# Optimization experiments

Measured on AMD Instinct MI355X. Metric: run time of the kernel, lower is better.

## Reference

```python
import math
import jax, jax.numpy as jnp
import numpy as np

BS, T, D_MODEL, H = 4, 1024, 1024, 16
D_K = D_MODEL // H


def setup_inputs() -> dict:
    key = jax.random.key(0)
    ks = jax.random.split(key, 16)
    s = 0.02  # weight init scale
    return {
        "q": jax.random.normal(ks[0], (BS, T, D_MODEL), jnp.float32),
        "k": jax.random.normal(ks[1], (BS, T, D_MODEL), jnp.float32),
        "v": jax.random.normal(ks[2], (BS, T, D_MODEL), jnp.float32),
        "pos_emb": jax.random.normal(ks[3], (1, T, D_MODEL), jnp.float32),
        "mask": jnp.ones((BS, T, T), jnp.int32),
        "Wq": jax.random.normal(ks[4], (D_MODEL, D_MODEL), jnp.float32) * s,
        "bq": jax.random.normal(ks[5], (D_MODEL,), jnp.float32) * s,
        "Wk": jax.random.normal(ks[6], (D_MODEL, D_MODEL), jnp.float32) * s,
        "bk": jax.random.normal(ks[7], (D_MODEL,), jnp.float32) * s,
        "Wv": jax.random.normal(ks[8], (D_MODEL, D_MODEL), jnp.float32) * s,
        "bv": jax.random.normal(ks[9], (D_MODEL,), jnp.float32) * s,
        "Wp": jax.random.normal(ks[10], (D_MODEL, D_MODEL), jnp.float32) * s,
        "pos_bias_u": jax.random.normal(ks[11], (H, D_K), jnp.float32) * s,
        "pos_bias_v": jax.random.normal(ks[12], (H, D_K), jnp.float32) * s,
        "Wo": jax.random.normal(ks[13], (D_MODEL, D_MODEL), jnp.float32) * s,
        "bo": jax.random.normal(ks[14], (D_MODEL,), jnp.float32) * s,
    }


def rel_shift(x):
    # x: [b, h, T, P]; Transformer-XL relative shift via pad+reshape
    b, h, t, p = x.shape
    x = jnp.pad(x, ((0, 0), (0, 0), (0, 0), (1, 0)))  # [b,h,T,P+1]
    x = x.reshape(b, h, p + 1, t)[:, :, 1:, :]
    return x.reshape(b, h, t, p)


def reference(q, k, v, pos_emb, mask, Wq, bq, Wk, bk, Wv, bv, Wp,
              pos_bias_u, pos_bias_v, Wo, bo):
    bs, t, d_model = q.shape
    h, d_k = pos_bias_u.shape
    # projections (torch Linear: x @ W.T + b)
    qh = (q @ Wq.T + bq).reshape(bs, t, h, d_k)                      # [b,t,h,d]
    kh = (k @ Wk.T + bk).reshape(bs, t, h, d_k).transpose(0, 2, 1, 3)  # [b,h,s,d]
    vh = (v @ Wv.T + bv).reshape(bs, t, h, d_k).transpose(0, 2, 1, 3)  # [b,h,s,d]
    p = (pos_emb @ Wp.T).reshape(pos_emb.shape[0], -1, h, d_k).transpose(0, 2, 1, 3)  # [1,h,P,d]
    q_u = (qh + pos_bias_u).transpose(0, 2, 1, 3)  # [b,h,t,d]
    q_v = (qh + pos_bias_v).transpose(0, 2, 1, 3)  # [b,h,t,d]
    matrix_ac = jnp.einsum('bhtd,bhsd->bhts', q_u, kh)
    matrix_bd = jnp.einsum('bhtd,hpd->bhtp', q_v, p[0])
    matrix_bd = rel_shift(matrix_bd)
    scores = (matrix_ac + matrix_bd) / math.sqrt(d_k)
    m = mask[:, None, :, :]  # broadcast over heads
    attn = jax.nn.softmax(jnp.where(m == 0, jnp.float32(-10000.0), scores), axis=-1)
    out_h = jnp.einsum('bhts,bhsd->bhtd', attn, vh)
    concat = out_h.transpose(0, 2, 1, 3).reshape(bs, t, d_model)
    output = concat @ Wo.T + bo
    return (output, attn)
```

## Files before the change

kernel.cpp:

```cpp
#include <hip/hip_runtime.h>

typedef _Float16 f16;
typedef __attribute__((ext_vector_type(8))) _Float16 f16x8;
typedef __attribute__((ext_vector_type(4))) float f32x4;

#define LDK 40
#define SST 1032
#define BST 72

__device__ __forceinline__ void stage_f16g(const f16* __restrict__ src, int ld, f16* dst) {
    int t = threadIdx.x;
    int row = t >> 2;
    int c0 = (t & 3) * 8;
    *(f16x8*)(dst + row * LDK + c0) = *(const f16x8*)(src + (size_t)row * ld + c0);
}

__device__ __forceinline__ void mma_step(const f16* As, const f16* Bs, int m_off, int n_off,
                                         f32x4 acc[2][2]) {
    int lane = threadIdx.x & 63;
    int r = lane & 15;
    int kq = (lane >> 4) * 8;
    f16x8 a0 = *(const f16x8*)(As + (m_off + r) * LDK + kq);
    f16x8 a1 = *(const f16x8*)(As + (m_off + 16 + r) * LDK + kq);
    f16x8 b0 = *(const f16x8*)(Bs + (n_off + r) * LDK + kq);
    f16x8 b1 = *(const f16x8*)(Bs + (n_off + 16 + r) * LDK + kq);
    acc[0][0] = __builtin_amdgcn_mfma_f32_16x16x32_f16(a0, b0, acc[0][0], 0, 0, 0);
    acc[0][1] = __builtin_amdgcn_mfma_f32_16x16x32_f16(a0, b1, acc[0][1], 0, 0, 0);
    acc[1][0] = __builtin_amdgcn_mfma_f32_16x16x32_f16(a1, b0, acc[1][0], 0, 0, 0);
    acc[1][1] = __builtin_amdgcn_mfma_f32_16x16x32_f16(a1, b1, acc[1][1], 0, 0, 0);
}

#define GEMM_PROLOGUE()                                         \
    __shared__ __align__(16) f16 As[64 * LDK];                  \
    __shared__ __align__(16) f16 Bs[64 * LDK];                  \
    const int w = threadIdx.x >> 6;                             \
    const int m_off = (w & 1) * 32, n_off = (w >> 1) * 32;      \
    const int lane = threadIdx.x & 63;                          \
    f32x4 zero = {0.f, 0.f, 0.f, 0.f};                          \
    f32x4 acc[2][2] = {{zero, zero}, {zero, zero}};

__global__ __launch_bounds__(256) void cvt_all(
    const float* __restrict__ q, const float* __restrict__ k, const float* __restrict__ v,
    const float* __restrict__ pe, const float* __restrict__ Wq, const float* __restrict__ Wk,
    const float* __restrict__ Wv, const float* __restrict__ Wp, const float* __restrict__ Wo,
    f16* __restrict__ dst) {
    const int seg = blockIdx.y;
    const float* srcs[9] = {q, k, v, pe, Wq, Wk, Wv, Wp, Wo};
    const int sz = (seg < 3) ? 4194304 : 1048576;
    const size_t off = (seg < 3) ? (size_t)seg * 4194304
                                 : (size_t)12582912 + (size_t)(seg - 3) * 1048576;
    const size_t i0 = ((size_t)blockIdx.x * 256 + threadIdx.x) * 16;
    if (i0 >= (size_t)sz) return;
    const float* s = srcs[seg] + i0;
    f16* d = dst + off + i0;
#pragma unroll
    for (int half = 0; half < 2; ++half) {
        float4 u = *(const float4*)(s + half * 8);
        float4 w = *(const float4*)(s + half * 8 + 4);
        f16x8 h;
        h[0] = (f16)u.x; h[1] = (f16)u.y; h[2] = (f16)u.z; h[3] = (f16)u.w;
        h[4] = (f16)w.x; h[5] = (f16)w.y; h[6] = (f16)w.z; h[7] = (f16)w.w;
        *(f16x8*)(d + half * 8) = h;
    }
}

__global__ __launch_bounds__(256) void proj_qkv(
    const f16* __restrict__ qf, const f16* __restrict__ kf, const f16* __restrict__ vf,
    const f16* __restrict__ Wqf, const f16* __restrict__ Wkf, const f16* __restrict__ Wvf,
    const float* __restrict__ bq, const float* __restrict__ bk, const float* __restrict__ bv,
    const float* __restrict__ pbu, const float* __restrict__ pbv,
    f16* __restrict__ q_u, f16* __restrict__ q_v, f16* __restrict__ kh,
    f16* __restrict__ vh) {
    GEMM_PROLOGUE();
    const int z = blockIdx.z;
    const f16* A = (z == 0) ? qf : (z == 1) ? kf : vf;
    const f16* W = (z == 0) ? Wqf : (z == 1) ? Wkf : Wvf;
    const float* bias = (z == 0) ? bq : (z == 1) ? bk : bv;
    const int m0 = blockIdx.y * 64, n0 = blockIdx.x * 64;
    for (int k0 = 0; k0 < 1024; k0 += 32) {
        stage_f16g(A + (size_t)m0 * 1024 + k0, 1024, As);
        stage_f16g(W + (size_t)n0 * 1024 + k0, 1024, Bs);
        __syncthreads();
        mma_step(As, Bs, m_off, n_off, acc);
        __syncthreads();
    }
#pragma unroll
    for (int mt = 0; mt < 2; ++mt)
#pragma unroll
        for (int nt = 0; nt < 2; ++nt)
#pragma unroll
            for (int rr = 0; rr < 4; ++rr) {
                int m = m0 + m_off + mt * 16 + (lane >> 4) * 4 + rr;
                int n = n0 + n_off + nt * 16 + (lane & 15);
                float base = acc[mt][nt][rr] + bias[n];
                int b = m >> 10, t = m & 1023, h = n >> 6, d = n & 63;
                size_t idx = ((size_t)((b * 16 + h) * 1024 + t)) * 64 + d;
                if (z == 0) {
                    q_u[idx] = (f16)(base + pbu[n]);
                    q_v[idx] = (f16)(base + pbv[n]);
                } else if (z == 1) {
                    kh[idx] = (f16)base;
                } else {
                    vh[idx] = (f16)base;
                }
            }
}

__global__ __launch_bounds__(256) void proj_p(const f16* __restrict__ A,
                                              const f16* __restrict__ W,
                                              f16* __restrict__ o1) {
    GEMM_PROLOGUE();
    const int m0 = blockIdx.y * 64;
    const int n0 = blockIdx.x * 64;
    for (int k0 = 0; k0 < 1024; k0 += 32) {
        stage_f16g(A + (size_t)m0 * 1024 + k0, 1024, As);
        stage_f16g(W + (size_t)n0 * 1024 + k0, 1024, Bs);
        __syncthreads();
        mma_step(As, Bs, m_off, n_off, acc);
        __syncthreads();
    }
#pragma unroll
    for (int mt = 0; mt < 2; ++mt)
#pragma unroll
        for (int nt = 0; nt < 2; ++nt)
#pragma unroll
            for (int rr = 0; rr < 4; ++rr) {
                int m = m0 + m_off + mt * 16 + (lane >> 4) * 4 + rr;
                int n = n0 + n_off + nt * 16 + (lane & 15);
                int h = n >> 6, d = n & 63;
                o1[((size_t)h * 1024 + m) * 64 + d] = (f16)acc[mt][nt][rr];
            }
}

__global__ __launch_bounds__(256) void transpose_v(const f16* __restrict__ vh,
                                                   f16* __restrict__ vT) {
    __shared__ __align__(16) f16 T[64 * BST];
    const int bh = blockIdx.y;
    const int j0 = blockIdx.x * 64;
    const int t = threadIdx.x;
    const int s = t >> 2, c0 = (t & 3) * 16;
    const f16* src = vh + (size_t)bh * 65536 + (size_t)(j0 + s) * 64;
    *(f16x8*)(T + s * BST + c0) = *(const f16x8*)(src + c0);
    *(f16x8*)(T + s * BST + c0 + 8) = *(const f16x8*)(src + c0 + 8);
    __syncthreads();
    const int d = t >> 2;
    f16x8 o0, o1;
#pragma unroll
    for (int j = 0; j < 8; ++j) {
        o0[j] = T[(c0 + j) * BST + d];
        o1[j] = T[(c0 + 8 + j) * BST + d];
    }
    f16* dst = vT + (size_t)bh * 65536 + (size_t)d * 1024 + j0 + c0;
    *(f16x8*)(dst) = o0;
    *(f16x8*)(dst + 8) = o1;
}

__global__ __launch_bounds__(256, 2) void fused_attn(
    const f16* __restrict__ q_u, const f16* __restrict__ q_v,
    const f16* __restrict__ kh, const f16* __restrict__ pp,
    const f16* __restrict__ vT, const int* __restrict__ mask,
    float* __restrict__ attn, f16* __restrict__ oh) {
    __shared__ __align__(16) f16 Ssc[32 * SST];
    __shared__ __align__(16) f16 Bt[64 * BST];
    __shared__ __align__(16) f16 rawX[1024];
    __shared__ __align__(16) f16 qxrow[64];

    const int bh = blockIdx.y;
    const int b = bh >> 4, h = bh & 15;
    const int i0 = blockIdx.x * 32;
    const int tid = threadIdx.x;
    const int w = tid >> 6;
    const int lane = tid & 63;
    const int m_off = (w & 1) * 16, n_off = (w >> 1) * 32;
    const int fr = lane & 15;
    const int kq = (lane >> 4) * 8;
    const f32x4 zero = {0.f, 0.f, 0.f, 0.f};

    const f16* Qu = q_u + (size_t)bh * 65536;
    const f16* Qv = q_v + (size_t)bh * 65536;
    const f16* Kh = kh + (size_t)bh * 65536;
    const f16* Pp = pp + (size_t)h * 65536;
    const f16* Vt = vT + (size_t)bh * 65536;

    f16x8 qu_f[2], qv_f[2];
#pragma unroll
    for (int ks = 0; ks < 2; ++ks) {
        size_t off = (size_t)(i0 + m_off + fr) * 64 + ks * 32 + kq;
        qu_f[ks] = *(const f16x8*)(Qu + off);
        qv_f[ks] = *(const f16x8*)(Qv + off);
    }
    if (i0 + 32 < 1024 && tid < 8)
        *(f16x8*)(qxrow + tid * 8) = *(const f16x8*)(Qv + (size_t)(i0 + 32) * 64 + tid * 8);

    const int srow = tid >> 2, sc0 = (tid & 3) * 16;
    for (int j0 = 0; j0 < 1024; j0 += 64) {
        {
            const f16* s = Pp + (size_t)(j0 + srow) * 64 + sc0;
            *(f16x8*)(Bt + srow * BST + sc0) = *(const f16x8*)(s);
            *(f16x8*)(Bt + srow * BST + sc0 + 8) = *(const f16x8*)(s + 8);
        }
        __syncthreads();
        f32x4 acc[2] = {zero, zero};
#pragma unroll
        for (int ks = 0; ks < 2; ++ks) {
            f16x8 b0 = *(const f16x8*)(Bt + (n_off + fr) * BST + ks * 32 + kq);
            f16x8 b1 = *(const f16x8*)(Bt + (n_off + 16 + fr) * BST + ks * 32 + kq);
            acc[0] = __builtin_amdgcn_mfma_f32_16x16x32_f16(qv_f[ks], b0, acc[0], 0, 0, 0);
            acc[1] = __builtin_amdgcn_mfma_f32_16x16x32_f16(qv_f[ks], b1, acc[1], 0, 0, 0);
        }
#pragma unroll
        for (int nt = 0; nt < 2; ++nt)
#pragma unroll
            for (int rr = 0; rr < 4; ++rr) {
                int m = m_off + (lane >> 4) * 4 + rr;
                int c = j0 + n_off + nt * 16 + fr;
                Ssc[m * SST + c] = (f16)acc[nt][rr];
            }
        __syncthreads();
    }

    if (i0 + 32 < 1024) {
        int p = tid * 4;
#pragma unroll
        for (int pi = 0; pi < 4; ++pi) {
            const f16* pr = Pp + (size_t)(p + pi) * 64;
            float sacc = 0.f;
#pragma unroll
            for (int c = 0; c < 64; c += 8) {
                f16x8 pv = *(const f16x8*)(pr + c);
                f16x8 qv8 = *(const f16x8*)(qxrow + c);
#pragma unroll
                for (int j = 0; j < 8; ++j) sacc += (float)pv[j] * (float)qv8[j];
            }
            rawX[p + pi] = (f16)sacc;
        }
    }
    __syncthreads();

    {
        const int s0 = lane * 16;
        f16 tmp[8][16];
#pragma unroll
        for (int rr2 = 0; rr2 < 8; ++rr2) {
            int lr = w * 8 + rr2;
            int r = i0 + lr;
#pragma unroll
            for (int j = 0; j < 16; ++j) {
                int s = s0 + j;
                f16 val;
                if (s <= r) val = Ssc[lr * SST + (s + 1023 - r)];
                else if (s == r + 1) val = (f16)0.f;
                else val = (lr == 31) ? rawX[s - r - 2] : Ssc[(lr + 1) * SST + (s - r - 2)];
                tmp[rr2][j] = val;
            }
        }
        __syncthreads();
#pragma unroll
        for (int rr2 = 0; rr2 < 8; ++rr2) {
            int lr = w * 8 + rr2;
            f16x8 o0, o1;
#pragma unroll
            for (int j = 0; j < 8; ++j) { o0[j] = tmp[rr2][j]; o1[j] = tmp[rr2][8 + j]; }
            *(f16x8*)(Ssc + lr * SST + s0) = o0;
            *(f16x8*)(Ssc + lr * SST + s0 + 8) = o1;
        }
    }
    __syncthreads();

    for (int j0 = 0; j0 < 1024; j0 += 64) {
        {
            const f16* s = Kh + (size_t)(j0 + srow) * 64 + sc0;
            *(f16x8*)(Bt + srow * BST + sc0) = *(const f16x8*)(s);
            *(f16x8*)(Bt + srow * BST + sc0 + 8) = *(const f16x8*)(s + 8);
        }
        __syncthreads();
        f32x4 acc[2] = {zero, zero};
#pragma unroll
        for (int ks = 0; ks < 2; ++ks) {
            f16x8 b0 = *(const f16x8*)(Bt + (n_off + fr) * BST + ks * 32 + kq);
            f16x8 b1 = *(const f16x8*)(Bt + (n_off + 16 + fr) * BST + ks * 32 + kq);
            acc[0] = __builtin_amdgcn_mfma_f32_16x16x32_f16(qu_f[ks], b0, acc[0], 0, 0, 0);
            acc[1] = __builtin_amdgcn_mfma_f32_16x16x32_f16(qu_f[ks], b1, acc[1], 0, 0, 0);
        }
#pragma unroll
        for (int nt = 0; nt < 2; ++nt)
#pragma unroll
            for (int rr = 0; rr < 4; ++rr) {
                int m = m_off + (lane >> 4) * 4 + rr;
                int c = j0 + n_off + nt * 16 + fr;
                float sc = ((float)Ssc[m * SST + c] + acc[nt][rr]) * 0.125f;
                Ssc[m * SST + c] = (f16)sc;
            }
        __syncthreads();
    }

    float* Ab = attn + (size_t)bh * 1048576;
    const int* MK = mask + ((size_t)b * 1024 + i0) * 1024;
    for (int rr = 0; rr < 8; ++rr) {
        int lr = w * 8 + rr;
        int c0 = lane * 16;
        f16x8 a0 = *(const f16x8*)(Ssc + lr * SST + c0);
        f16x8 a1 = *(const f16x8*)(Ssc + lr * SST + c0 + 8);
        const int* mrow = MK + (size_t)lr * 1024 + c0;
        int4 mk0 = *(const int4*)mrow;
        int4 mk1 = *(const int4*)(mrow + 4);
        int4 mk2 = *(const int4*)(mrow + 8);
        int4 mk3 = *(const int4*)(mrow + 12);
        int mks[16] = {mk0.x, mk0.y, mk0.z, mk0.w, mk1.x, mk1.y, mk1.z, mk1.w,
                       mk2.x, mk2.y, mk2.z, mk2.w, mk3.x, mk3.y, mk3.z, mk3.w};
        float vals[16];
        float mx = -1e30f;
#pragma unroll
        for (int j = 0; j < 16; ++j) {
            float v = (j < 8) ? (float)a0[j] : (float)a1[j - 8];
            if (mks[j] == 0) v = -10000.0f;
            vals[j] = v;
            mx = fmaxf(mx, v);
        }
#pragma unroll
        for (int off = 32; off > 0; off >>= 1) mx = fmaxf(mx, __shfl_xor(mx, off));
        float sum = 0.f;
#pragma unroll
        for (int j = 0; j < 16; ++j) { vals[j] = __expf(vals[j] - mx); sum += vals[j]; }
#pragma unroll
        for (int off = 32; off > 0; off >>= 1) sum += __shfl_xor(sum, off);
        float il = 1.f / sum;
        float* arow = Ab + (size_t)(i0 + lr) * 1024 + c0;
        float4 f0 = {vals[0] * il, vals[1] * il, vals[2] * il, vals[3] * il};
        float4 f1 = {vals[4] * il, vals[5] * il, vals[6] * il, vals[7] * il};
        float4 f2 = {vals[8] * il, vals[9] * il, vals[10] * il, vals[11] * il};
        float4 f3 = {vals[12] * il, vals[13] * il, vals[14] * il, vals[15] * il};
        *(float4*)(arow) = f0;
        *(float4*)(arow + 4) = f1;
        *(float4*)(arow + 8) = f2;
        *(float4*)(arow + 12) = f3;
        f16x8 p0, p1;
#pragma unroll
        for (int j = 0; j < 8; ++j) {
            p0[j] = (f16)(vals[j] * il);
            p1[j] = (f16)(vals[8 + j] * il);
        }
        *(f16x8*)(Ssc + lr * SST + c0) = p0;
        *(f16x8*)(Ssc + lr * SST + c0 + 8) = p1;
    }

    f32x4 accp[2] = {zero, zero};
    for (int j0 = 0; j0 < 1024; j0 += 64) {
        {
            const f16* s = Vt + (size_t)srow * 1024 + j0 + sc0;
            *(f16x8*)(Bt + srow * BST + sc0) = *(const f16x8*)(s);
            *(f16x8*)(Bt + srow * BST + sc0 + 8) = *(const f16x8*)(s + 8);
        }
        __syncthreads();
#pragma unroll
        for (int ks = 0; ks < 2; ++ks) {
            f16x8 a0 = *(const f16x8*)(Ssc + (m_off + fr) * SST + j0 + ks * 32 + kq);
            f16x8 b0 = *(const f16x8*)(Bt + (n_off + fr) * BST + ks * 32 + kq);
            f16x8 b1 = *(const f16x8*)(Bt + (n_off + 16 + fr) * BST + ks * 32 + kq);
            accp[0] = __builtin_amdgcn_mfma_f32_16x16x32_f16(a0, b0, accp[0], 0, 0, 0);
            accp[1] = __builtin_amdgcn_mfma_f32_16x16x32_f16(a0, b1, accp[1], 0, 0, 0);
        }
        __syncthreads();
    }
#pragma unroll
    for (int nt = 0; nt < 2; ++nt)
#pragma unroll
        for (int rr = 0; rr < 4; ++rr) {
            int t = i0 + m_off + (lane >> 4) * 4 + rr;
            int d = n_off + nt * 16 + fr;
            oh[((size_t)(b * 1024 + t)) * 1024 + h * 64 + d] = (f16)accp[nt][rr];
        }
}

__global__ __launch_bounds__(256) void out_gemm(const f16* __restrict__ A,
                                                const f16* __restrict__ W,
                                                const float* __restrict__ bias,
                                                float* __restrict__ out) {
    GEMM_PROLOGUE();
    const int m0 = blockIdx.y * 64;
    const int n0 = blockIdx.x * 64;
    for (int k0 = 0; k0 < 1024; k0 += 32) {
        stage_f16g(A + (size_t)m0 * 1024 + k0, 1024, As);
        stage_f16g(W + (size_t)n0 * 1024 + k0, 1024, Bs);
        __syncthreads();
        mma_step(As, Bs, m_off, n_off, acc);
        __syncthreads();
    }
#pragma unroll
    for (int mt = 0; mt < 2; ++mt)
#pragma unroll
        for (int nt = 0; nt < 2; ++nt)
#pragma unroll
            for (int rr = 0; rr < 4; ++rr) {
                int m = m0 + m_off + mt * 16 + (lane >> 4) * 4 + rr;
                int n = n0 + n_off + nt * 16 + (lane & 15);
                out[(size_t)m * 1024 + n] = acc[mt][nt][rr] + bias[n];
            }
}

extern "C" void kernel_launch(void* const* d_in, const int* in_sizes, int n_in,
                              void* d_out, int out_size, void* d_ws, size_t ws_size,
                              hipStream_t stream) {
    (void)in_sizes; (void)n_in; (void)out_size; (void)ws_size;
    const float* q   = (const float*)d_in[0];
    const float* k   = (const float*)d_in[1];
    const float* v   = (const float*)d_in[2];
    const float* pe  = (const float*)d_in[3];
    const int*   msk = (const int*)d_in[4];
    const float* Wq  = (const float*)d_in[5];
    const float* bq  = (const float*)d_in[6];
    const float* Wk  = (const float*)d_in[7];
    const float* bk  = (const float*)d_in[8];
    const float* Wv  = (const float*)d_in[9];
    const float* bv  = (const float*)d_in[10];
    const float* Wp  = (const float*)d_in[11];
    const float* pbu = (const float*)d_in[12];
    const float* pbv = (const float*)d_in[13];
    const float* Wo  = (const float*)d_in[14];
    const float* bo  = (const float*)d_in[15];

    char* ws = (char*)d_ws;
    f16* cvt = (f16*)(ws + 0);
    f16* qf  = cvt;
    f16* kf  = cvt + 4194304;
    f16* vf  = cvt + 8388608;
    f16* pef = cvt + 12582912;
    f16* Wqf = cvt + 13631488;
    f16* Wkf = cvt + 14680064;
    f16* Wvf = cvt + 15728640;
    f16* Wpf = cvt + 16777216;
    f16* Wof = cvt + 17825792;

    f16* q_u = (f16*)(ws + 37748736);
    f16* q_v = (f16*)(ws + 46137344);
    f16* kh  = (f16*)(ws + 54525952);
    f16* vh  = (f16*)(ws + 62914560);
    f16* pp  = (f16*)(ws + 71303168);
    f16* oh  = (f16*)(ws + 73400320);
    f16* vT  = (f16*)(ws + 81788928);

    float* out  = (float*)d_out;
    float* attn = out + 4194304;

    dim3 blk(256);
    cvt_all<<<dim3(1024, 9), blk, 0, stream>>>(q, k, v, pe, Wq, Wk, Wv, Wp, Wo, cvt);
    proj_qkv<<<dim3(16, 64, 3), blk, 0, stream>>>(qf, kf, vf, Wqf, Wkf, Wvf, bq, bk, bv,
                                                  pbu, pbv, q_u, q_v, kh, vh);
    proj_p<<<dim3(16, 16), blk, 0, stream>>>(pef, Wpf, pp);
    transpose_v<<<dim3(16, 64), blk, 0, stream>>>(vh, vT);
    fused_attn<<<dim3(32, 64), blk, 0, stream>>>(q_u, q_v, kh, pp, vT, msk, attn, oh);
    out_gemm<<<dim3(16, 64), blk, 0, stream>>>(oh, Wof, bo, out);
}
```

Before: 684.8 us.

## Register-prefetch GEMM tiles and fold rel_shift into score scatter

Adds register double-buffering to all GEMM k-loops and to the P, K and V tile loops in the attention kernel, so the next global tile load is issued before the current MFMA step. It also scatters the positional scores directly into their rel-shifted positions, replacing the separate gather pass, its extra barriers and the rawX buffer. Softmax column mapping changes to two strided halves per lane for better LDS and global coalescing. The shifted-scatter indexing is intricate and could hide correctness edge cases.

```diff
diff --git a/kernel.cpp b/kernel.cpp
--- a/kernel.cpp
+++ b/kernel.cpp
@@ -8,11 +8,17 @@
 #define SST 1032
 #define BST 72
 
-__device__ __forceinline__ void stage_f16g(const f16* __restrict__ src, int ld, f16* dst) {
+__device__ __forceinline__ f16x8 ld_half(const f16* __restrict__ src, int ld) {
     int t = threadIdx.x;
     int row = t >> 2;
     int c0 = (t & 3) * 8;
-    *(f16x8*)(dst + row * LDK + c0) = *(const f16x8*)(src + (size_t)row * ld + c0);
+    return *(const f16x8*)(src + (size_t)row * ld + c0);
+}
+__device__ __forceinline__ void st_half(f16* dst, f16x8 v) {
+    int t = threadIdx.x;
+    int row = t >> 2;
+    int c0 = (t & 3) * 8;
+    *(f16x8*)(dst + row * LDK + c0) = v;
 }
 
 __device__ __forceinline__ void mma_step(const f16* As, const f16* Bs, int m_off, int n_off,
@@ -38,6 +44,23 @@
     const int lane = threadIdx.x & 63;                          \
     f32x4 zero = {0.f, 0.f, 0.f, 0.f};                          \
     f32x4 acc[2][2] = {{zero, zero}, {zero, zero}};
+
+#define GEMM_KLOOP(Abase, Wbase)                                        \
+    {                                                                   \
+        f16x8 ra = ld_half((Abase), 1024);                              \
+        f16x8 rb = ld_half((Wbase), 1024);                              \
+        for (int k0 = 0; k0 < 1024; k0 += 32) {                         \
+            st_half(As, ra);                                            \
+            st_half(Bs, rb);                                            \
+            __syncthreads();                                            \
+            if (k0 + 32 < 1024) {                                       \
+                ra = ld_half((Abase) + k0 + 32, 1024);                  \
+                rb = ld_half((Wbase) + k0 + 32, 1024);                  \
+            }                                                           \
+            mma_step(As, Bs, m_off, n_off, acc);                        \
+            __syncthreads();                                            \
+        }                                                               \
+    }
 
 __global__ __launch_bounds__(256) void cvt_all(
     const float* __restrict__ q, const float* __restrict__ k, const float* __restrict__ v,
@@ -77,13 +100,7 @@
     const f16* W = (z == 0) ? Wqf : (z == 1) ? Wkf : Wvf;
     const float* bias = (z == 0) ? bq : (z == 1) ? bk : bv;
     const int m0 = blockIdx.y * 64, n0 = blockIdx.x * 64;
-    for (int k0 = 0; k0 < 1024; k0 += 32) {
-        stage_f16g(A + (size_t)m0 * 1024 + k0, 1024, As);
-        stage_f16g(W + (size_t)n0 * 1024 + k0, 1024, Bs);
-        __syncthreads();
-        mma_step(As, Bs, m_off, n_off, acc);
-        __syncthreads();
-    }
+    GEMM_KLOOP(A + (size_t)m0 * 1024, W + (size_t)n0 * 1024);
 #pragma unroll
     for (int mt = 0; mt < 2; ++mt)
 #pragma unroll
@@ -112,13 +129,7 @@
     GEMM_PROLOGUE();
     const int m0 = blockIdx.y * 64;
     const int n0 = blockIdx.x * 64;
-    for (int k0 = 0; k0 < 1024; k0 += 32) {
-        stage_f16g(A + (size_t)m0 * 1024 + k0, 1024, As);
-        stage_f16g(W + (size_t)n0 * 1024 + k0, 1024, Bs);
-        __syncthreads();
-        mma_step(As, Bs, m_off, n_off, acc);
-        __syncthreads();
-    }
+    GEMM_KLOOP(A + (size_t)m0 * 1024, W + (size_t)n0 * 1024);
 #pragma unroll
     for (int mt = 0; mt < 2; ++mt)
 #pragma unroll
@@ -162,7 +173,6 @@
     float* __restrict__ attn, f16* __restrict__ oh) {
     __shared__ __align__(16) f16 Ssc[32 * SST];
     __shared__ __align__(16) f16 Bt[64 * BST];
-    __shared__ __align__(16) f16 rawX[1024];
     __shared__ __align__(16) f16 qxrow[64];
 
     const int bh = blockIdx.y;
@@ -193,119 +203,127 @@
         *(f16x8*)(qxrow + tid * 8) = *(const f16x8*)(Qv + (size_t)(i0 + 32) * 64 + tid * 8);
 
     const int srow = tid >> 2, sc0 = (tid & 3) * 16;
-    for (int j0 = 0; j0 < 1024; j0 += 64) {
+
+    {
+        f16x8 pf0, pf1;
         {
-            const f16* s = Pp + (size_t)(j0 + srow) * 64 + sc0;
-            *(f16x8*)(Bt + srow * BST + sc0) = *(const f16x8*)(s);
-            *(f16x8*)(Bt + srow * BST + sc0 + 8) = *(const f16x8*)(s + 8);
-        }
-        __syncthreads();
-        f32x4 acc[2] = {zero, zero};
-#pragma unroll
-        for (int ks = 0; ks < 2; ++ks) {
-            f16x8 b0 = *(const f16x8*)(Bt + (n_off + fr) * BST + ks * 32 + kq);
-            f16x8 b1 = *(const f16x8*)(Bt + (n_off + 16 + fr) * BST + ks * 32 + kq);
-            acc[0] = __builtin_amdgcn_mfma_f32_16x16x32_f16(qv_f[ks], b0, acc[0], 0, 0, 0);
-            acc[1] = __builtin_amdgcn_mfma_f32_16x16x32_f16(qv_f[ks], b1, acc[1], 0, 0, 0);
-        }
-#pragma unroll
-        for (int nt = 0; nt < 2; ++nt)
-#pragma unroll
-            for (int rr = 0; rr < 4; ++rr) {
-                int m = m_off + (lane >> 4) * 4 + rr;
-                int c = j0 + n_off + nt * 16 + fr;
-                Ssc[m * SST + c] = (f16)acc[nt][rr];
-            }
-        __syncthreads();
+            const f16* s = Pp + (size_t)srow * 64 + sc0;
+            pf0 = *(const f16x8*)(s);
+            pf1 = *(const f16x8*)(s + 8);
+        }
+        for (int j0 = 0; j0 < 1024; j0 += 64) {
+            *(f16x8*)(Bt + srow * BST + sc0) = pf0;
+            *(f16x8*)(Bt + srow * BST + sc0 + 8) = pf1;
+            __syncthreads();
+            if (j0 + 64 < 1024) {
+                const f16* s = Pp + (size_t)(j0 + 64 + srow) * 64 + sc0;
+                pf0 = *(const f16x8*)(s);
+                pf1 = *(const f16x8*)(s + 8);
+            }
+            f32x4 acc[2] = {zero, zero};
+#pragma unroll
+            for (int ks = 0; ks < 2; ++ks) {
+                f16x8 b0 = *(const f16x8*)(Bt + (n_off + fr) * BST + ks * 32 + kq);
+                f16x8 b1 = *(const f16x8*)(Bt + (n_off + 16 + fr) * BST + ks * 32 + kq);
+                acc[0] = __builtin_amdgcn_mfma_f32_16x16x32_f16(qv_f[ks], b0, acc[0], 0, 0, 0);
+                acc[1] = __builtin_amdgcn_mfma_f32_16x16x32_f16(qv_f[ks], b1, acc[1], 0, 0, 0);
+            }
+#pragma unroll
+            for (int nt = 0; nt < 2; ++nt)
+#pragma unroll
+                for (int rr = 0; rr < 4; ++rr) {
+                    int m = m_off + (lane >> 4) * 4 + rr;
+                    int p = j0 + n_off + nt * 16 + fr;
+                    int pr = p + i0 + m;
+                    f16 v = (f16)acc[nt][rr];
+                    if (pr >= 1023) {
+                        Ssc[m * SST + (pr - 1023)] = v;
+                    } else if (m > 0) {
+                        Ssc[(m - 1) * SST + (pr + 1)] = v;
+                    }
+                }
+            __syncthreads();
+        }
+    }
+
+    if (tid < 32) {
+        int c = i0 + tid + 1;
+        if (c < 1024) Ssc[tid * SST + c] = (f16)0.f;
     }
 
     if (i0 + 32 < 1024) {
-        int p = tid * 4;
-#pragma unroll
-        for (int pi = 0; pi < 4; ++pi) {
-            const f16* pr = Pp + (size_t)(p + pi) * 64;
-            float sacc = 0.f;
-#pragma unroll
-            for (int c = 0; c < 64; c += 8) {
-                f16x8 pv = *(const f16x8*)(pr + c);
-                f16x8 qv8 = *(const f16x8*)(qxrow + c);
-#pragma unroll
-                for (int j = 0; j < 8; ++j) sacc += (float)pv[j] * (float)qv8[j];
-            }
-            rawX[p + pi] = (f16)sacc;
-        }
-    }
-    __syncthreads();
+        int base = tid * 4;
+        if (base + i0 + 33 <= 1023) {
+#pragma unroll
+            for (int pi = 0; pi < 4; ++pi) {
+                int p = base + pi;
+                int s = p + i0 + 33;
+                if (s <= 1023) {
+                    const f16* pr = Pp + (size_t)p * 64;
+                    float sacc = 0.f;
+#pragma unroll
+                    for (int c = 0; c < 64; c += 8) {
+                        f16x8 pv = *(const f16x8*)(pr + c);
+                        f16x8 qv8 = *(const f16x8*)(qxrow + c);
+#pragma unroll
+                        for (int j = 0; j < 8; ++j) sacc += (float)pv[j] * (float)qv8[j];
+                    }
+                    Ssc[31 * SST + s] = (f16)sacc;
+                }
+            }
+        }
+    }
 
     {
-        const int s0 = lane * 16;
-        f16 tmp[8][16];
-#pragma unroll
-        for (int rr2 = 0; rr2 < 8; ++rr2) {
-            int lr = w * 8 + rr2;
-            int r = i0 + lr;
-#pragma unroll
-            for (int j = 0; j < 16; ++j) {
-                int s = s0 + j;
-                f16 val;
-                if (s <= r) val = Ssc[lr * SST + (s + 1023 - r)];
-                else if (s == r + 1) val = (f16)0.f;
-                else val = (lr == 31) ? rawX[s - r - 2] : Ssc[(lr + 1) * SST + (s - r - 2)];
-                tmp[rr2][j] = val;
-            }
-        }
-        __syncthreads();
-#pragma unroll
-        for (int rr2 = 0; rr2 < 8; ++rr2) {
-            int lr = w * 8 + rr2;
-            f16x8 o0, o1;
-#pragma unroll
-            for (int j = 0; j < 8; ++j) { o0[j] = tmp[rr2][j]; o1[j] = tmp[rr2][8 + j]; }
-            *(f16x8*)(Ssc + lr * SST + s0) = o0;
-            *(f16x8*)(Ssc + lr * SST + s0 + 8) = o1;
-        }
-    }
-    __syncthreads();
-
-    for (int j0 = 0; j0 < 1024; j0 += 64) {
+        f16x8 pf0, pf1;
         {
-            const f16* s = Kh + (size_t)(j0 + srow) * 64 + sc0;
-            *(f16x8*)(Bt + srow * BST + sc0) = *(const f16x8*)(s);
-            *(f16x8*)(Bt + srow * BST + sc0 + 8) = *(const f16x8*)(s + 8);
-        }
-        __syncthreads();
-        f32x4 acc[2] = {zero, zero};
-#pragma unroll
-        for (int ks = 0; ks < 2; ++ks) {
-            f16x8 b0 = *(const f16x8*)(Bt + (n_off + fr) * BST + ks * 32 + kq);
-            f16x8 b1 = *(const f16x8*)(Bt + (n_off + 16 + fr) * BST + ks * 32 + kq);
-            acc[0] = __builtin_amdgcn_mfma_f32_16x16x32_f16(qu_f[ks], b0, acc[0], 0, 0, 0);
-            acc[1] = __builtin_amdgcn_mfma_f32_16x16x32_f16(qu_f[ks], b1, acc[1], 0, 0, 0);
-        }
-#pragma unroll
-        for (int nt = 0; nt < 2; ++nt)
-#pragma unroll
-            for (int rr = 0; rr < 4; ++rr) {
-                int m = m_off + (lane >> 4) * 4 + rr;
-                int c = j0 + n_off + nt * 16 + fr;
-                float sc = ((float)Ssc[m * SST + c] + acc[nt][rr]) * 0.125f;
-                Ssc[m * SST + c] = (f16)sc;
-            }
-        __syncthreads();
+            const f16* s = Kh + (size_t)srow * 64 + sc0;
+            pf0 = *(const f16x8*)(s);
+            pf1 = *(const f16x8*)(s + 8);
+        }
+        for (int j0 = 0; j0 < 1024; j0 += 64) {
+            *(f16x8*)(Bt + srow * BST + sc0) = pf0;
+            *(f16x8*)(Bt + srow * BST + sc0 + 8) = pf1;
+            __syncthreads();
+            if (j0 + 64 < 1024) {
+                const f16* s = Kh + (size_t)(j0 + 64 + srow) * 64 + sc0;
+                pf0 = *(const f16x8*)(s);
+                pf1 = *(const f16x8*)(s + 8);
+            }
+            f32x4 acc[2] = {zero, zero};
+#pragma unroll
+            for (int ks = 0; ks < 2; ++ks) {
+                f16x8 b0 = *(const f16x8*)(Bt + (n_off + fr) * BST + ks * 32 + kq);
+                f16x8 b1 = *(const f16x8*)(Bt + (n_off + 16 + fr) * BST + ks * 32 + kq);
+                acc[0] = __builtin_amdgcn_mfma_f32_16x16x32_f16(qu_f[ks], b0, acc[0], 0, 0, 0);
+                acc[1] = __builtin_amdgcn_mfma_f32_16x16x32_f16(qu_f[ks], b1, acc[1], 0, 0, 0);
+            }
+#pragma unroll
+            for (int nt = 0; nt < 2; ++nt)
+#pragma unroll
+                for (int rr = 0; rr < 4; ++rr) {
+                    int m = m_off + (lane >> 4) * 4 + rr;
+                    int c = j0 + n_off + nt * 16 + fr;
+                    float sc = ((float)Ssc[m * SST + c] + acc[nt][rr]) * 0.125f;
+                    Ssc[m * SST + c] = (f16)sc;
+                }
+            __syncthreads();
+        }
     }
 
     float* Ab = attn + (size_t)bh * 1048576;
     const int* MK = mask + ((size_t)b * 1024 + i0) * 1024;
     for (int rr = 0; rr < 8; ++rr) {
         int lr = w * 8 + rr;
-        int c0 = lane * 16;
+        int c0 = lane * 8;
+        int c1 = 512 + lane * 8;
         f16x8 a0 = *(const f16x8*)(Ssc + lr * SST + c0);
-        f16x8 a1 = *(const f16x8*)(Ssc + lr * SST + c0 + 8);
-        const int* mrow = MK + (size_t)lr * 1024 + c0;
-        int4 mk0 = *(const int4*)mrow;
-        int4 mk1 = *(const int4*)(mrow + 4);
-        int4 mk2 = *(const int4*)(mrow + 8);
-        int4 mk3 = *(const int4*)(mrow + 12);
+        f16x8 a1 = *(const f16x8*)(Ssc + lr * SST + c1);
+        const int* mrow = MK + (size_t)lr * 1024;
+        int4 mk0 = *(const int4*)(mrow + c0);
+        int4 mk1 = *(const int4*)(mrow + c0 + 4);
+        int4 mk2 = *(const int4*)(mrow + c1);
+        int4 mk3 = *(const int4*)(mrow + c1 + 4);
         int mks[16] = {mk0.x, mk0.y, mk0.z, mk0.w, mk1.x, mk1.y, mk1.z, mk1.w,
                        mk2.x, mk2.y, mk2.z, mk2.w, mk3.x, mk3.y, mk3.z, mk3.w};
         float vals[16];
@@ -325,15 +343,15 @@
 #pragma unroll
         for (int off = 32; off > 0; off >>= 1) sum += __shfl_xor(sum, off);
         float il = 1.f / sum;
-        float* arow = Ab + (size_t)(i0 + lr) * 1024 + c0;
+        float* arow = Ab + (size_t)(i0 + lr) * 1024;
         float4 f0 = {vals[0] * il, vals[1] * il, vals[2] * il, vals[3] * il};
         float4 f1 = {vals[4] * il, vals[5] * il, vals[6] * il, vals[7] * il};
         float4 f2 = {vals[8] * il, vals[9] * il, vals[10] * il, vals[11] * il};
         float4 f3 = {vals[12] * il, vals[13] * il, vals[14] * il, vals[15] * il};
-        *(float4*)(arow) = f0;
-        *(float4*)(arow + 4) = f1;
-        *(float4*)(arow + 8) = f2;
-        *(float4*)(arow + 12) = f3;
+        *(float4*)(arow + c0) = f0;
+        *(float4*)(arow + c0 + 4) = f1;
+        *(float4*)(arow + c1) = f2;
+        *(float4*)(arow + c1 + 4) = f3;
         f16x8 p0, p1;
 #pragma unroll
         for (int j = 0; j < 8; ++j) {
@@ -341,26 +359,36 @@
             p1[j] = (f16)(vals[8 + j] * il);
         }
         *(f16x8*)(Ssc + lr * SST + c0) = p0;
-        *(f16x8*)(Ssc + lr * SST + c0 + 8) = p1;
+        *(f16x8*)(Ssc + lr * SST + c1) = p1;
     }
 
     f32x4 accp[2] = {zero, zero};
-    for (int j0 = 0; j0 < 1024; j0 += 64) {
+    {
+        f16x8 pf0, pf1;
         {
-            const f16* s = Vt + (size_t)srow * 1024 + j0 + sc0;
-            *(f16x8*)(Bt + srow * BST + sc0) = *(const f16x8*)(s);
-            *(f16x8*)(Bt + srow * BST + sc0 + 8) = *(const f16x8*)(s + 8);
-        }
-        __syncthreads();
-#pragma unroll
-        for (int ks = 0; ks < 2; ++ks) {
-            f16x8 a0 = *(const f16x8*)(Ssc + (m_off + fr) * SST + j0 + ks * 32 + kq);
-            f16x8 b0 = *(const f16x8*)(Bt + (n_off + fr) * BST + ks * 32 + kq);
-            f16x8 b1 = *(const f16x8*)(Bt + (n_off + 16 + fr) * BST + ks * 32 + kq);
-            accp[0] = __builtin_amdgcn_mfma_f32_16x16x32_f16(a0, b0, accp[0], 0, 0, 0);
-            accp[1] = __builtin_amdgcn_mfma_f32_16x16x32_f16(a0, b1, accp[1], 0, 0, 0);
-        }
-        __syncthreads();
+            const f16* s = Vt + (size_t)srow * 1024 + sc0;
+            pf0 = *(const f16x8*)(s);
+            pf1 = *(const f16x8*)(s + 8);
+        }
+        for (int j0 = 0; j0 < 1024; j0 += 64) {
+            *(f16x8*)(Bt + srow * BST + sc0) = pf0;
+            *(f16x8*)(Bt + srow * BST + sc0 + 8) = pf1;
+            __syncthreads();
+            if (j0 + 64 < 1024) {
+                const f16* s = Vt + (size_t)srow * 1024 + j0 + 64 + sc0;
+                pf0 = *(const f16x8*)(s);
+                pf1 = *(const f16x8*)(s + 8);
+            }
+#pragma unroll
+            for (int ks = 0; ks < 2; ++ks) {
+                f16x8 a0 = *(const f16x8*)(Ssc + (m_off + fr) * SST + j0 + ks * 32 + kq);
+                f16x8 b0 = *(const f16x8*)(Bt + (n_off + fr) * BST + ks * 32 + kq);
+                f16x8 b1 = *(const f16x8*)(Bt + (n_off + 16 + fr) * BST + ks * 32 + kq);
+                accp[0] = __builtin_amdgcn_mfma_f32_16x16x32_f16(a0, b0, accp[0], 0, 0, 0);
+                accp[1] = __builtin_amdgcn_mfma_f32_16x16x32_f16(a0, b1, accp[1], 0, 0, 0);
+            }
+            __syncthreads();
+        }
     }
 #pragma unroll
     for (int nt = 0; nt < 2; ++nt)
@@ -379,13 +407,7 @@
     GEMM_PROLOGUE();
     const int m0 = blockIdx.y * 64;
     const int n0 = blockIdx.x * 64;
-    for (int k0 = 0; k0 < 1024; k0 += 32) {
-        stage_f16g(A + (size_t)m0 * 1024 + k0, 1024, As);
-        stage_f16g(W + (size_t)n0 * 1024 + k0, 1024, Bs);
-        __syncthreads();
-        mma_step(As, Bs, m_off, n_off, acc);
-        __syncthreads();
-    }
+    GEMM_KLOOP(A + (size_t)m0 * 1024, W + (size_t)n0 * 1024);
 #pragma unroll
     for (int mt = 0; mt < 2; ++mt)
 #pragma unroll
```

Result: faster. 602.2 us (-12.1%).
